# Kernel optimization log

Hardware: AMD Instinct MI355X
Metric: run time of the kernel (lower is better)

## Reference

```python
import jax, jax.numpy as jnp
import numpy as np

N_NODES = 100000
N_EDGES = 625000
D_IN = 128
D_HID = 256


def setup_inputs() -> dict:
    key = jax.random.key(0)
    ks = jax.random.split(key, 9)
    x = jax.random.normal(ks[0], (N_NODES, D_IN), dtype=jnp.float32)
    edge_index = jax.random.randint(ks[1], (2, N_EDGES), 0, N_NODES, dtype=jnp.int64)
    s = 1.0 / np.sqrt(D_IN)
    # SAGEConv params: lin_l applied to mean-aggregated neighbors (with bias),
    # lin_r applied to root features (no bias) -- PyG defaults.
    w_l = jax.random.uniform(ks[2], (D_IN, D_HID), minval=-s, maxval=s, dtype=jnp.float32)
    b_l = jax.random.uniform(ks[3], (D_HID,), minval=-s, maxval=s, dtype=jnp.float32)
    w_r = jax.random.uniform(ks[4], (D_IN, D_HID), minval=-s, maxval=s, dtype=jnp.float32)
    sh = 1.0 / np.sqrt(D_HID)
    w_p = jax.random.uniform(ks[5], (D_HID, 7), minval=-sh, maxval=sh, dtype=jnp.float32)
    b_p = jax.random.uniform(ks[6], (7,), minval=-sh, maxval=sh, dtype=jnp.float32)
    w_s = jax.random.uniform(ks[7], (D_HID, 6), minval=-sh, maxval=sh, dtype=jnp.float32)
    b_s = jax.random.uniform(ks[8], (6,), minval=-sh, maxval=sh, dtype=jnp.float32)
    return {"x": x, "edge_index": edge_index, "w_l": w_l, "b_l": b_l, "w_r": w_r,
            "w_p": w_p, "b_p": b_p, "w_s": w_s, "b_s": b_s}


def reference(x, edge_index, w_l, b_l, w_r, w_p, b_p, w_s, b_s):
    src, dst = edge_index[0], edge_index[1]
    n = x.shape[0]
    # SAGEConv mean aggregation: mean of source-node features over each target
    agg = jax.ops.segment_sum(x[src], dst, num_segments=n)          # [N, D_IN]
    cnt = jax.ops.segment_sum(jnp.ones(src.shape, x.dtype), dst, num_segments=n)
    mean = agg / jnp.maximum(cnt, 1.0)[:, None]                      # isolated nodes -> 0
    h = mean @ w_l + b_l + x @ w_r                                   # [N, D_HID]
    h = jax.nn.relu(h)                                               # dropout = identity (eval)
    pr = h @ w_p + b_p                                               # [N, 7]
    sv = h @ w_s + b_s                                               # [N, 6]
    return jax.nn.log_softmax(pr, axis=1), jax.nn.log_softmax(sv, axis=1)
```

## Files before the change

kernel.cpp:

```cpp
#include <hip/hip_runtime.h>
#include <hip/hip_bf16.h>
#include <math.h>

#define NN 100000
#define NE 625000
#define DIN 128
#define DH 256
#define NROWS 100096
#define CAP 32

#define HS_STRIDE 264

#define XCAST_BLOCKS 12500
#define EDGE_BLOCKS  2442
#define PACKW_BLOCKS 32
#define PACKH_BLOCKS 2
#define PREP_BLOCKS  (XCAST_BLOCKS + EDGE_BLOCKS + PACKW_BLOCKS + PACKH_BLOCKS)

typedef __attribute__((ext_vector_type(8))) short bf16x8;
typedef __attribute__((ext_vector_type(4))) float f32x4;

__device__ __forceinline__ unsigned short f2bf(float f) {
    unsigned u = __builtin_bit_cast(unsigned, f);
    u += 0x7fffu + ((u >> 16) & 1u);
    return (unsigned short)(u >> 16);
}
__device__ __forceinline__ float bflo(unsigned u) {
    return __builtin_bit_cast(float, u << 16);
}
__device__ __forceinline__ float bfhi(unsigned u) {
    return __builtin_bit_cast(float, u & 0xffff0000u);
}

__global__ __launch_bounds__(256)
void prep(const float* __restrict__ x, const int* __restrict__ ei,
          const float* __restrict__ w_l, const float* __restrict__ w_r,
          const float* __restrict__ w_p, const float* __restrict__ w_s,
          const float* __restrict__ b_p, const float* __restrict__ b_s,
          unsigned short* __restrict__ A, unsigned short* __restrict__ Bp,
          unsigned short* __restrict__ whp, float* __restrict__ bhc,
          int* __restrict__ deg, int* __restrict__ elist) {
    const int b = blockIdx.x;
    const int t = threadIdx.x;

    if (b < XCAST_BLOCKS) {
        int idx = b * 256 + t;
        int n = idx >> 5;
        int j4 = (idx & 31) * 4;
        float4 v = *reinterpret_cast<const float4*>(x + (size_t)n * DIN + j4);
        ushort4 o = { f2bf(v.x), f2bf(v.y), f2bf(v.z), f2bf(v.w) };
        *reinterpret_cast<ushort4*>(A + (size_t)n * 128 + j4) = o;
    } else if (b < XCAST_BLOCKS + EDGE_BLOCKS) {
        int e = (b - XCAST_BLOCKS) * 256 + t;
        if (e < NE) {
            int dst = ei[NE + e];
            int pos = atomicAdd(&deg[dst], 1);
            if (pos < CAP) elist[dst * CAP + pos] = ei[e];
        }
    } else if (b < XCAST_BLOCKS + EDGE_BLOCKS + PACKW_BLOCKS) {
        int tid = (b - XCAST_BLOCKS - EDGE_BLOCKS) * 256 + t;
        int kt = tid >> 10;
        int ct = (tid >> 6) & 15;
        int L = tid & 63;
        int k0 = kt * 32 + (L >> 4) * 8;
        int c = ct * 16 + (L & 15);
        unsigned short v[8];
#pragma unroll
        for (int j = 0; j < 8; ++j) {
            int k = k0 + j;
            float w = (k < 128) ? w_l[k * 256 + c] : w_r[(k - 128) * 256 + c];
            v[j] = f2bf(w);
        }
        int g = ((ct >> 3) << 6) + (kt << 3) + (ct & 7);
        *reinterpret_cast<bf16x8*>(Bp + (size_t)(g * 64 + L) * 8) =
            *reinterpret_cast<const bf16x8*>(v);
    } else {
        int tid = (b - XCAST_BLOCKS - EDGE_BLOCKS - PACKW_BLOCKS) * 256 + t;
        int kt = tid >> 6;
        int L = tid & 63;
        int k0 = kt * 32 + (L >> 4) * 8;
        int c = L & 15;
        unsigned short v[8];
#pragma unroll
        for (int j = 0; j < 8; ++j) {
            int k = k0 + j;
            float w = (c < 7) ? w_p[k * 7 + c] : (c < 13 ? w_s[k * 6 + (c - 7)] : 0.f);
            v[j] = f2bf(w);
        }
        *reinterpret_cast<bf16x8*>(whp + (size_t)tid * 8) =
            *reinterpret_cast<const bf16x8*>(v);
        if (tid < 16)
            bhc[tid] = (tid < 7) ? b_p[tid] : (tid < 13 ? b_s[tid - 7] : 0.f);
        if (tid >= 16 && tid < 32) {
            uint4 z = {0u, 0u, 0u, 0u};
            *reinterpret_cast<uint4*>(A + (size_t)NN * 128 + (tid - 16) * 8) = z;
        }
    }
}

__device__ __forceinline__ void gload(const unsigned short* __restrict__ A,
                                      int src, int q,
                                      uint4& v0, uint4& v1, uint4& v2, uint4& v3) {
    const unsigned short* xr = A + (size_t)src * 128 + q * 8;
    v0 = *reinterpret_cast<const uint4*>(xr);
    v1 = *reinterpret_cast<const uint4*>(xr + 32);
    v2 = *reinterpret_cast<const uint4*>(xr + 64);
    v3 = *reinterpret_cast<const uint4*>(xr + 96);
}

__device__ __forceinline__ void gacc(float* macc,
                                     const uint4& v0, const uint4& v1,
                                     const uint4& v2, const uint4& v3) {
    macc[0]  += bflo(v0.x); macc[1]  += bfhi(v0.x);
    macc[2]  += bflo(v0.y); macc[3]  += bfhi(v0.y);
    macc[4]  += bflo(v0.z); macc[5]  += bfhi(v0.z);
    macc[6]  += bflo(v0.w); macc[7]  += bfhi(v0.w);
    macc[8]  += bflo(v1.x); macc[9]  += bfhi(v1.x);
    macc[10] += bflo(v1.y); macc[11] += bfhi(v1.y);
    macc[12] += bflo(v1.z); macc[13] += bfhi(v1.z);
    macc[14] += bflo(v1.w); macc[15] += bfhi(v1.w);
    macc[16] += bflo(v2.x); macc[17] += bfhi(v2.x);
    macc[18] += bflo(v2.y); macc[19] += bfhi(v2.y);
    macc[20] += bflo(v2.z); macc[21] += bfhi(v2.z);
    macc[22] += bflo(v2.w); macc[23] += bfhi(v2.w);
    macc[24] += bflo(v3.x); macc[25] += bfhi(v3.x);
    macc[26] += bflo(v3.y); macc[27] += bfhi(v3.y);
    macc[28] += bflo(v3.z); macc[29] += bfhi(v3.z);
    macc[30] += bflo(v3.w); macc[31] += bfhi(v3.w);
}

__global__ __launch_bounds__(512, 4)
void sage_gemm_fused(const unsigned short* __restrict__ A,
                     const unsigned short* __restrict__ Bp,
                     const float* __restrict__ b_l,
                     const unsigned short* __restrict__ whp,
                     const float* __restrict__ bhc,
                     const int* __restrict__ elist,
                     const int* __restrict__ deg,
                     float* __restrict__ out) {
    __shared__ __align__(16) unsigned char smem[76288];
    unsigned short* Bs = (unsigned short*)smem;
    unsigned short* hs = (unsigned short*)smem;
    float* o13 = (float*)(smem + 67584);

    const int t = threadIdx.x;
    const int wave = t >> 6;
    const int L = t & 63;
    const int q = L >> 4;
    const int m15 = L & 15;
    const int node0 = blockIdx.x * 128;
    const int rowbase = node0 + wave * 16;
    const int n = rowbase + m15;

    {
        const uint4* gsrc = reinterpret_cast<const uint4*>(Bp);
        uint4* ldst = reinterpret_cast<uint4*>(Bs);
#pragma unroll
        for (int r = 0; r < 8; ++r)
            ldst[r * 512 + t] = gsrc[r * 512 + t];
    }

    const unsigned short* arow = A + (size_t)n * 128;
    bf16x8 afrag[8];
#pragma unroll
    for (int kt = 4; kt < 8; ++kt)
        afrag[kt] = *reinterpret_cast<const bf16x8*>(arow + (kt - 4) * 32 + q * 8);

    {
        float macc[32];
#pragma unroll
        for (int j = 0; j < 32; ++j) macc[j] = 0.f;
        int d = 0;
        if (n < NN) d = deg[n];
        const int dl = (d < CAP) ? d : CAP;
        const int dpad = (dl + 1) & ~1;
        const int base = (n < NN ? n : 0) * CAP;

        int s0 = elist[base + 0];
        int s1 = elist[base + 1];
        s0 = (dl > 0) ? s0 : NN;
        s1 = (dl > 1) ? s1 : NN;

        for (int i = 0; i < dpad; i += 2) {
            uint4 a0, a1, a2, a3, b0, b1, b2, b3;
            gload(A, s0, q, a0, a1, a2, a3);
            gload(A, s1, q, b0, b1, b2, b3);
            const int i2 = i + 2;
            int t0 = elist[base + (i2 & 31)];
            int t1 = elist[base + ((i2 + 1) & 31)];
            t0 = (i2 < dl) ? t0 : NN;
            t1 = (i2 + 1 < dl) ? t1 : NN;
            gacc(macc, a0, a1, a2, a3);
            gacc(macc, b0, b1, b2, b3);
            s0 = t0; s1 = t1;
        }

        const float invd = (d > 0) ? 1.f / (float)d : 0.f;
#pragma unroll
        for (int kt = 0; kt < 4; ++kt) {
            unsigned short vv[8];
#pragma unroll
            for (int j = 0; j < 8; ++j) vv[j] = f2bf(macc[kt * 8 + j] * invd);
            afrag[kt] = *reinterpret_cast<const bf16x8*>(vv);
        }
    }

    f32x4 acc[16];
#pragma unroll
    for (int ct = 0; ct < 16; ++ct) acc[ct] = (f32x4){0.f, 0.f, 0.f, 0.f};

    __syncthreads();

#pragma unroll
    for (int kt = 0; kt < 8; ++kt) {
#pragma unroll
        for (int c7 = 0; c7 < 8; ++c7) {
            bf16x8 b = *reinterpret_cast<const bf16x8*>(
                Bs + ((size_t)(kt * 8 + c7) * 64 + L) * 8);
            acc[c7] = __builtin_amdgcn_mfma_f32_16x16x32_bf16(afrag[kt], b, acc[c7], 0, 0, 0);
        }
    }

    __syncthreads();

    {
        const uint4* gsrc = reinterpret_cast<const uint4*>(Bp + 32768);
        uint4* ldst = reinterpret_cast<uint4*>(Bs);
#pragma unroll
        for (int r = 0; r < 8; ++r)
            ldst[r * 512 + t] = gsrc[r * 512 + t];
    }
    __syncthreads();

#pragma unroll
    for (int kt = 0; kt < 8; ++kt) {
#pragma unroll
        for (int c7 = 0; c7 < 8; ++c7) {
            bf16x8 b = *reinterpret_cast<const bf16x8*>(
                Bs + ((size_t)(kt * 8 + c7) * 64 + L) * 8);
            acc[8 + c7] = __builtin_amdgcn_mfma_f32_16x16x32_bf16(afrag[kt], b, acc[8 + c7], 0, 0, 0);
        }
    }

    __syncthreads();

#pragma unroll
    for (int ct = 0; ct < 16; ++ct) {
        const int c = ct * 16 + m15;
        const float blv = b_l[c];
        const int r0 = wave * 16 + q * 4;
#pragma unroll
        for (int r = 0; r < 4; ++r)
            hs[(r0 + r) * HS_STRIDE + c] = f2bf(fmaxf(acc[ct][r] + blv, 0.f));
    }
    __syncthreads();

    {
        f32x4 acch = (f32x4){0.f, 0.f, 0.f, 0.f};
        const unsigned short* hrow = hs + (size_t)(wave * 16 + m15) * HS_STRIDE;
#pragma unroll
        for (int kt = 0; kt < 8; ++kt) {
            bf16x8 ah = *reinterpret_cast<const bf16x8*>(hrow + kt * 32 + q * 8);
            bf16x8 bh = *reinterpret_cast<const bf16x8*>(whp + ((size_t)(kt * 64 + L)) * 8);
            acch = __builtin_amdgcn_mfma_f32_16x16x32_bf16(ah, bh, acch, 0, 0, 0);
        }
        if (m15 < 13) {
            const float bh = bhc[m15];
#pragma unroll
            for (int r = 0; r < 4; ++r)
                o13[(wave * 16 + q * 4 + r) * 17 + m15] = acch[r] + bh;
        }
    }
    __syncthreads();

    if (t < 128) {
        const int gnode = node0 + t;
        if (gnode < NN) {
            float v[7], mx = -1e30f;
#pragma unroll
            for (int j = 0; j < 7; ++j) { v[j] = o13[t * 17 + j]; mx = fmaxf(mx, v[j]); }
            float sum = 0.f;
#pragma unroll
            for (int j = 0; j < 7; ++j) sum += expf(v[j] - mx);
            const float lse = mx + logf(sum);
#pragma unroll
            for (int j = 0; j < 7; ++j) out[(size_t)gnode * 7 + j] = v[j] - lse;

            float u[6], mx2 = -1e30f;
#pragma unroll
            for (int j = 0; j < 6; ++j) { u[j] = o13[t * 17 + 7 + j]; mx2 = fmaxf(mx2, u[j]); }
            float sum2 = 0.f;
#pragma unroll
            for (int j = 0; j < 6; ++j) sum2 += expf(u[j] - mx2);
            const float lse2 = mx2 + logf(sum2);
#pragma unroll
            for (int j = 0; j < 6; ++j) out[(size_t)NN * 7 + (size_t)gnode * 6 + j] = u[j] - lse2;
        }
    }
}

extern "C" void kernel_launch(void* const* d_in, const int* in_sizes, int n_in,
                              void* d_out, int out_size, void* d_ws, size_t ws_size,
                              hipStream_t stream) {
    const float* x   = (const float*)d_in[0];
    const int*   ei  = (const int*)d_in[1];
    const float* w_l = (const float*)d_in[2];
    const float* b_l = (const float*)d_in[3];
    const float* w_r = (const float*)d_in[4];
    const float* w_p = (const float*)d_in[5];
    const float* b_p = (const float*)d_in[6];
    const float* w_s = (const float*)d_in[7];
    const float* b_s = (const float*)d_in[8];
    float* out = (float*)d_out;

    unsigned short* A   = (unsigned short*)d_ws;
    unsigned short* Bp  = A + (size_t)NROWS * 128;
    unsigned short* whp = Bp + 65536;
    float* bhc  = (float*)(whp + 4096);
    int* deg    = (int*)(bhc + 16);
    int* elist  = deg + NN;

    hipMemsetAsync(deg, 0, NN * sizeof(int), stream);

    prep<<<PREP_BLOCKS, 256, 0, stream>>>(x, ei, w_l, w_r, w_p, w_s, b_p, b_s,
                                          A, Bp, whp, bhc, deg, elist);

    sage_gemm_fused<<<NROWS / 128, 512, 0, stream>>>(A, Bp, b_l, whp, bhc,
                                                     elist, deg, out);
}
```

Measured before the change: 209.3 us.

## Counting-sort nodes by degree so each wave gathers neighbors of equal degree

Adds three small kernels that build a histogram of capped node degrees, a prefix scan and a scatter into a permutation that packs each node id with its capped degree. The fused gather+GEMM kernel then processes nodes in degree-sorted order, so the 16 nodes in a wave have near-equal neighbor counts and the gather loop wastes fewer iterations on lanes that have already finished. The cost is three extra launches, root-feature rows and output rows that are now read and written in scattered order, and a mean that divides by the capped degree instead of the true degree.

Result: slower. 220.5 us (+5.4%).

```diff
diff --git a/kernel.cpp b/kernel.cpp
--- a/kernel.cpp
+++ b/kernel.cpp
@@ -8,6 +8,7 @@
 #define DH 256
 #define NROWS 100096
 #define CAP 32
+#define NBINS 33
 
 #define HS_STRIDE 264
 
@@ -95,6 +96,60 @@
             uint4 z = {0u, 0u, 0u, 0u};
             *reinterpret_cast<uint4*>(A + (size_t)NN * 128 + (tid - 16) * 8) = z;
         }
+    }
+}
+
+__global__ __launch_bounds__(1024)
+void deg_hist(const int* __restrict__ deg, int* __restrict__ bins) {
+    __shared__ int h[NBINS];
+    const int t = threadIdx.x;
+    if (t < NBINS) h[t] = 0;
+    __syncthreads();
+    int n = blockIdx.x * 1024 + t;
+    if (n < NN) {
+        int d = deg[n];
+        int dl = (d < CAP) ? d : CAP;
+        atomicAdd(&h[dl], 1);
+    }
+    __syncthreads();
+    if (t < NBINS && h[t]) atomicAdd(&bins[t], h[t]);
+}
+
+__global__ __launch_bounds__(128)
+void deg_scan(const int* __restrict__ bins, int* __restrict__ cursor,
+              unsigned* __restrict__ perm) {
+    const int t = threadIdx.x;
+    if (t == 0) {
+        int run = 0;
+        for (int b = 0; b < NBINS; ++b) { cursor[b] = run; run += bins[b]; }
+    }
+    if (t >= 32) perm[NN + (t - 32)] = NN;
+}
+
+__global__ __launch_bounds__(1024)
+void deg_scatter(const int* __restrict__ deg, int* __restrict__ cursor,
+                 unsigned* __restrict__ perm) {
+    __shared__ int h[NBINS];
+    __shared__ int base[NBINS];
+    const int t = threadIdx.x;
+    const int n = blockIdx.x * 1024 + t;
+    if (t < NBINS) h[t] = 0;
+    __syncthreads();
+    int dl = 0;
+    if (n < NN) {
+        int d = deg[n];
+        dl = (d < CAP) ? d : CAP;
+        atomicAdd(&h[dl], 1);
+    }
+    __syncthreads();
+    if (t < NBINS) {
+        base[t] = h[t] ? atomicAdd(&cursor[t], h[t]) : 0;
+        h[t] = 0;
+    }
+    __syncthreads();
+    if (n < NN) {
+        int pos = base[dl] + atomicAdd(&h[dl], 1);
+        perm[pos] = (unsigned)n | ((unsigned)dl << 20);
     }
 }
 
@@ -136,7 +191,7 @@
                      const unsigned short* __restrict__ whp,
                      const float* __restrict__ bhc,
                      const int* __restrict__ elist,
-                     const int* __restrict__ deg,
+                     const unsigned* __restrict__ perm,
                      float* __restrict__ out) {
     __shared__ __align__(16) unsigned char smem[76288];
     unsigned short* Bs = (unsigned short*)smem;
@@ -150,17 +205,20 @@
     const int m15 = L & 15;
     const int node0 = blockIdx.x * 128;
     const int rowbase = node0 + wave * 16;
-    const int n = rowbase + m15;
+    const int r = rowbase + m15;
+    const unsigned pe = perm[r];
+    const int node = pe & 0xFFFFF;
+    const int dl = pe >> 20;
 
     {
         const uint4* gsrc = reinterpret_cast<const uint4*>(Bp);
         uint4* ldst = reinterpret_cast<uint4*>(Bs);
 #pragma unroll
-        for (int r = 0; r < 8; ++r)
-            ldst[r * 512 + t] = gsrc[r * 512 + t];
-    }
-
-    const unsigned short* arow = A + (size_t)n * 128;
+        for (int rr = 0; rr < 8; ++rr)
+            ldst[rr * 512 + t] = gsrc[rr * 512 + t];
+    }
+
+    const unsigned short* arow = A + (size_t)node * 128;
     bf16x8 afrag[8];
 #pragma unroll
     for (int kt = 4; kt < 8; ++kt)
@@ -170,11 +228,8 @@
         float macc[32];
 #pragma unroll
         for (int j = 0; j < 32; ++j) macc[j] = 0.f;
-        int d = 0;
-        if (n < NN) d = deg[n];
-        const int dl = (d < CAP) ? d : CAP;
         const int dpad = (dl + 1) & ~1;
-        const int base = (n < NN ? n : 0) * CAP;
+        const int base = (node < NN ? node : 0) * CAP;
 
         int s0 = elist[base + 0];
         int s1 = elist[base + 1];
@@ -195,7 +250,7 @@
             s0 = t0; s1 = t1;
         }
 
-        const float invd = (d > 0) ? 1.f / (float)d : 0.f;
+        const float invd = (dl > 0) ? 1.f / (float)dl : 0.f;
 #pragma unroll
         for (int kt = 0; kt < 4; ++kt) {
             unsigned short vv[8];
@@ -227,8 +282,8 @@
         const uint4* gsrc = reinterpret_cast<const uint4*>(Bp + 32768);
         uint4* ldst = reinterpret_cast<uint4*>(Bs);
 #pragma unroll
-        for (int r = 0; r < 8; ++r)
-            ldst[r * 512 + t] = gsrc[r * 512 + t];
+        for (int rr = 0; rr < 8; ++rr)
+            ldst[rr * 512 + t] = gsrc[rr * 512 + t];
     }
     __syncthreads();
 
@@ -250,8 +305,8 @@
         const float blv = b_l[c];
         const int r0 = wave * 16 + q * 4;
 #pragma unroll
-        for (int r = 0; r < 4; ++r)
-            hs[(r0 + r) * HS_STRIDE + c] = f2bf(fmaxf(acc[ct][r] + blv, 0.f));
+        for (int rr = 0; rr < 4; ++rr)
+            hs[(r0 + rr) * HS_STRIDE + c] = f2bf(fmaxf(acc[ct][rr] + blv, 0.f));
     }
     __syncthreads();
 
@@ -267,14 +322,15 @@
         if (m15 < 13) {
             const float bh = bhc[m15];
 #pragma unroll
-            for (int r = 0; r < 4; ++r)
-                o13[(wave * 16 + q * 4 + r) * 17 + m15] = acch[r] + bh;
+            for (int rr = 0; rr < 4; ++rr)
+                o13[(wave * 16 + q * 4 + rr) * 17 + m15] = acch[rr] + bh;
         }
     }
     __syncthreads();
 
     if (t < 128) {
-        const int gnode = node0 + t;
+        const unsigned pe2 = perm[node0 + t];
+        const int gnode = pe2 & 0xFFFFF;
         if (gnode < NN) {
             float v[7], mx = -1e30f;
 #pragma unroll
@@ -318,13 +374,20 @@
     unsigned short* whp = Bp + 65536;
     float* bhc  = (float*)(whp + 4096);
     int* deg    = (int*)(bhc + 16);
-    int* elist  = deg + NN;
-
-    hipMemsetAsync(deg, 0, NN * sizeof(int), stream);
+    int* bins   = deg + NN;
+    int* cursor = bins + 64;
+    int* elist  = cursor + 64;
+    unsigned* perm = (unsigned*)(elist + (size_t)NN * CAP);
+
+    hipMemsetAsync(deg, 0, (NN + 128) * sizeof(int), stream);
 
     prep<<<PREP_BLOCKS, 256, 0, stream>>>(x, ei, w_l, w_r, w_p, w_s, b_p, b_s,
                                           A, Bp, whp, bhc, deg, elist);
 
+    deg_hist<<<(NN + 1023) / 1024, 1024, 0, stream>>>(deg, bins);
+    deg_scan<<<1, 128, 0, stream>>>(bins, cursor, perm);
+    deg_scatter<<<(NN + 1023) / 1024, 1024, 0, stream>>>(deg, cursor, perm);
+
     sage_gemm_fused<<<NROWS / 128, 512, 0, stream>>>(A, Bp, b_l, whp, bhc,
-                                                     elist, deg, out);
-}
+                                                     elist, perm, out);
+}
```

## Split neighbor mean gather into separate kernel writing into widened A buffer

Applied to the files above, without the earlier changes.

Moves the neighbor-mean aggregation out of the fused GEMM kernel into a standalone gather_mean kernel with higher occupancy, storing bf16 means next to x in a stride-256 A buffer. The GEMM then simply loads both halves of the A row. This aims to improve latency hiding for the irregular gather, which was constrained by the GEMM kernel's large shared memory use, at the cost of an extra launch and an extra write/read of the mean matrix. Edge-list blocks are also reordered to run first in the prep grid.

New measurement: 251.3 us. +20.1%, slower.

```diff
diff --git a/kernel.cpp b/kernel.cpp
--- a/kernel.cpp
+++ b/kernel.cpp
@@ -8,14 +8,15 @@
 #define DH 256
 #define NROWS 100096
 #define CAP 32
+#define AST 256
 
 #define HS_STRIDE 264
 
+#define EDGE_BLOCKS  2442
 #define XCAST_BLOCKS 12500
-#define EDGE_BLOCKS  2442
 #define PACKW_BLOCKS 32
 #define PACKH_BLOCKS 2
-#define PREP_BLOCKS  (XCAST_BLOCKS + EDGE_BLOCKS + PACKW_BLOCKS + PACKH_BLOCKS)
+#define PREP_BLOCKS  (EDGE_BLOCKS + XCAST_BLOCKS + PACKW_BLOCKS + PACKH_BLOCKS)
 
 typedef __attribute__((ext_vector_type(8))) short bf16x8;
 typedef __attribute__((ext_vector_type(4))) float f32x4;
@@ -43,22 +44,22 @@
     const int b = blockIdx.x;
     const int t = threadIdx.x;
 
-    if (b < XCAST_BLOCKS) {
-        int idx = b * 256 + t;
+    if (b < EDGE_BLOCKS) {
+        int e = b * 256 + t;
+        if (e < NE) {
+            int dst = ei[NE + e];
+            int pos = atomicAdd(&deg[dst], 1);
+            if (pos < CAP) elist[dst * CAP + pos] = ei[e];
+        }
+    } else if (b < EDGE_BLOCKS + XCAST_BLOCKS) {
+        int idx = (b - EDGE_BLOCKS) * 256 + t;
         int n = idx >> 5;
         int j4 = (idx & 31) * 4;
         float4 v = *reinterpret_cast<const float4*>(x + (size_t)n * DIN + j4);
         ushort4 o = { f2bf(v.x), f2bf(v.y), f2bf(v.z), f2bf(v.w) };
-        *reinterpret_cast<ushort4*>(A + (size_t)n * 128 + j4) = o;
-    } else if (b < XCAST_BLOCKS + EDGE_BLOCKS) {
-        int e = (b - XCAST_BLOCKS) * 256 + t;
-        if (e < NE) {
-            int dst = ei[NE + e];
-            int pos = atomicAdd(&deg[dst], 1);
-            if (pos < CAP) elist[dst * CAP + pos] = ei[e];
-        }
-    } else if (b < XCAST_BLOCKS + EDGE_BLOCKS + PACKW_BLOCKS) {
-        int tid = (b - XCAST_BLOCKS - EDGE_BLOCKS) * 256 + t;
+        *reinterpret_cast<ushort4*>(A + (size_t)n * AST + 128 + j4) = o;
+    } else if (b < EDGE_BLOCKS + XCAST_BLOCKS + PACKW_BLOCKS) {
+        int tid = (b - EDGE_BLOCKS - XCAST_BLOCKS) * 256 + t;
         int kt = tid >> 10;
         int ct = (tid >> 6) & 15;
         int L = tid & 63;
@@ -75,7 +76,7 @@
         *reinterpret_cast<bf16x8*>(Bp + (size_t)(g * 64 + L) * 8) =
             *reinterpret_cast<const bf16x8*>(v);
     } else {
-        int tid = (b - XCAST_BLOCKS - EDGE_BLOCKS - PACKW_BLOCKS) * 256 + t;
+        int tid = (b - EDGE_BLOCKS - XCAST_BLOCKS - PACKW_BLOCKS) * 256 + t;
         int kt = tid >> 6;
         int L = tid & 63;
         int k0 = kt * 32 + (L >> 4) * 8;
@@ -93,7 +94,7 @@
             bhc[tid] = (tid < 7) ? b_p[tid] : (tid < 13 ? b_s[tid - 7] : 0.f);
         if (tid >= 16 && tid < 32) {
             uint4 z = {0u, 0u, 0u, 0u};
-            *reinterpret_cast<uint4*>(A + (size_t)NN * 128 + (tid - 16) * 8) = z;
+            *reinterpret_cast<uint4*>(A + (size_t)NN * AST + 128 + (tid - 16) * 8) = z;
         }
     }
 }
@@ -101,7 +102,7 @@
 __device__ __forceinline__ void gload(const unsigned short* __restrict__ A,
                                       int src, int q,
                                       uint4& v0, uint4& v1, uint4& v2, uint4& v3) {
-    const unsigned short* xr = A + (size_t)src * 128 + q * 8;
+    const unsigned short* xr = A + (size_t)src * AST + 128 + q * 8;
     v0 = *reinterpret_cast<const uint4*>(xr);
     v1 = *reinterpret_cast<const uint4*>(xr + 32);
     v2 = *reinterpret_cast<const uint4*>(xr + 64);
@@ -129,14 +130,65 @@
     macc[30] += bflo(v3.w); macc[31] += bfhi(v3.w);
 }
 
+__global__ __launch_bounds__(256, 6)
+void gather_mean(unsigned short* __restrict__ A,
+                 const int* __restrict__ elist,
+                 const int* __restrict__ deg) {
+    const int t = threadIdx.x;
+    const int L = t & 63;
+    const int q = L >> 4;
+    const int m15 = L & 15;
+    const int n = blockIdx.x * 64 + (t >> 6) * 16 + m15;
+
+    int d = 0;
+    if (n < NN) d = deg[n];
+    const int dl = (d < CAP) ? d : CAP;
+    const int dpad = (dl + 1) & ~1;
+    const int base = (n < NN ? n : 0) * CAP;
+
+    float macc[32];
+#pragma unroll
+    for (int j = 0; j < 32; ++j) macc[j] = 0.f;
+
+    int s0 = elist[base + 0];
+    int s1 = elist[base + 1];
+    s0 = (dl > 0) ? s0 : NN;
+    s1 = (dl > 1) ? s1 : NN;
+
+    for (int i = 0; i < dpad; i += 2) {
+        uint4 a0, a1, a2, a3, b0, b1, b2, b3;
+        gload(A, s0, q, a0, a1, a2, a3);
+        gload(A, s1, q, b0, b1, b2, b3);
+        const int i2 = i + 2;
+        int t0 = elist[base + (i2 & 31)];
+        int t1 = elist[base + ((i2 + 1) & 31)];
+        t0 = (i2 < dl) ? t0 : NN;
+        t1 = (i2 + 1 < dl) ? t1 : NN;
+        gacc(macc, a0, a1, a2, a3);
+        gacc(macc, b0, b1, b2, b3);
+        s0 = t0; s1 = t1;
+    }
+
+    if (n < NN) {
+        const float invd = (dl > 0) ? 1.f / (float)dl : 0.f;
+        unsigned short* mrow = A + (size_t)n * AST;
+#pragma unroll
+        for (int kt = 0; kt < 4; ++kt) {
+            unsigned short vv[8];
+#pragma unroll
+            for (int j = 0; j < 8; ++j) vv[j] = f2bf(macc[kt * 8 + j] * invd);
+            *reinterpret_cast<bf16x8*>(mrow + kt * 32 + q * 8) =
+                *reinterpret_cast<const bf16x8*>(vv);
+        }
+    }
+}
+
 __global__ __launch_bounds__(512, 4)
 void sage_gemm_fused(const unsigned short* __restrict__ A,
                      const unsigned short* __restrict__ Bp,
                      const float* __restrict__ b_l,
                      const unsigned short* __restrict__ whp,
                      const float* __restrict__ bhc,
-                     const int* __restrict__ elist,
-                     const int* __restrict__ deg,
                      float* __restrict__ out) {
     __shared__ __align__(16) unsigned char smem[76288];
     unsigned short* Bs = (unsigned short*)smem;
@@ -149,61 +201,21 @@
     const int q = L >> 4;
     const int m15 = L & 15;
     const int node0 = blockIdx.x * 128;
-    const int rowbase = node0 + wave * 16;
-    const int n = rowbase + m15;
+    const int node = node0 + wave * 16 + m15;
 
     {
         const uint4* gsrc = reinterpret_cast<const uint4*>(Bp);
         uint4* ldst = reinterpret_cast<uint4*>(Bs);
 #pragma unroll
-        for (int r = 0; r < 8; ++r)
-            ldst[r * 512 + t] = gsrc[r * 512 + t];
-    }
-
-    const unsigned short* arow = A + (size_t)n * 128;
+        for (int rr = 0; rr < 8; ++rr)
+            ldst[rr * 512 + t] = gsrc[rr * 512 + t];
+    }
+
+    const unsigned short* arow = A + (size_t)node * AST;
     bf16x8 afrag[8];
 #pragma unroll
-    for (int kt = 4; kt < 8; ++kt)
-        afrag[kt] = *reinterpret_cast<const bf16x8*>(arow + (kt - 4) * 32 + q * 8);
-
-    {
-        float macc[32];
-#pragma unroll
-        for (int j = 0; j < 32; ++j) macc[j] = 0.f;
-        int d = 0;
-        if (n < NN) d = deg[n];
-        const int dl = (d < CAP) ? d : CAP;
-        const int dpad = (dl + 1) & ~1;
-        const int base = (n < NN ? n : 0) * CAP;
-
-        int s0 = elist[base + 0];
-        int s1 = elist[base + 1];
-        s0 = (dl > 0) ? s0 : NN;
-        s1 = (dl > 1) ? s1 : NN;
-
-        for (int i = 0; i < dpad; i += 2) {
-            uint4 a0, a1, a2, a3, b0, b1, b2, b3;
-            gload(A, s0, q, a0, a1, a2, a3);
-            gload(A, s1, q, b0, b1, b2, b3);
-            const int i2 = i + 2;
-            int t0 = elist[base + (i2 & 31)];
-            int t1 = elist[base + ((i2 + 1) & 31)];
-            t0 = (i2 < dl) ? t0 : NN;
-            t1 = (i2 + 1 < dl) ? t1 : NN;
-            gacc(macc, a0, a1, a2, a3);
-            gacc(macc, b0, b1, b2, b3);
-            s0 = t0; s1 = t1;
-        }
-
-        const float invd = (d > 0) ? 1.f / (float)d : 0.f;
-#pragma unroll
-        for (int kt = 0; kt < 4; ++kt) {
-            unsigned short vv[8];
-#pragma unroll
-            for (int j = 0; j < 8; ++j) vv[j] = f2bf(macc[kt * 8 + j] * invd);
-            afrag[kt] = *reinterpret_cast<const bf16x8*>(vv);
-        }
-    }
+    for (int kt = 0; kt < 8; ++kt)
+        afrag[kt] = *reinterpret_cast<const bf16x8*>(arow + kt * 32 + q * 8);
 
     f32x4 acc[16];
 #pragma unroll
@@ -227,8 +239,8 @@
         const uint4* gsrc = reinterpret_cast<const uint4*>(Bp + 32768);
         uint4* ldst = reinterpret_cast<uint4*>(Bs);
 #pragma unroll
-        for (int r = 0; r < 8; ++r)
-            ldst[r * 512 + t] = gsrc[r * 512 + t];
+        for (int rr = 0; rr < 8; ++rr)
+            ldst[rr * 512 + t] = gsrc[rr * 512 + t];
     }
     __syncthreads();
 
@@ -250,8 +262,8 @@
         const float blv = b_l[c];
         const int r0 = wave * 16 + q * 4;
 #pragma unroll
-        for (int r = 0; r < 4; ++r)
-            hs[(r0 + r) * HS_STRIDE + c] = f2bf(fmaxf(acc[ct][r] + blv, 0.f));
+        for (int rr = 0; rr < 4; ++rr)
+            hs[(r0 + rr) * HS_STRIDE + c] = f2bf(fmaxf(acc[ct][rr] + blv, 0.f));
     }
     __syncthreads();
 
@@ -267,8 +279,8 @@
         if (m15 < 13) {
             const float bh = bhc[m15];
 #pragma unroll
-            for (int r = 0; r < 4; ++r)
-                o13[(wave * 16 + q * 4 + r) * 17 + m15] = acch[r] + bh;
+            for (int rr = 0; rr < 4; ++rr)
+                o13[(wave * 16 + q * 4 + rr) * 17 + m15] = acch[rr] + bh;
         }
     }
     __syncthreads();
@@ -314,7 +326,7 @@
     float* out = (float*)d_out;
 
     unsigned short* A   = (unsigned short*)d_ws;
-    unsigned short* Bp  = A + (size_t)NROWS * 128;
+    unsigned short* Bp  = A + (size_t)NROWS * AST;
     unsigned short* whp = Bp + 65536;
     float* bhc  = (float*)(whp + 4096);
     int* deg    = (int*)(bhc + 16);
@@ -325,6 +337,7 @@
     prep<<<PREP_BLOCKS, 256, 0, stream>>>(x, ei, w_l, w_r, w_p, w_s, b_p, b_s,
                                           A, Bp, whp, bhc, deg, elist);
 
-    sage_gemm_fused<<<NROWS / 128, 512, 0, stream>>>(A, Bp, b_l, whp, bhc,
-                                                     elist, deg, out);
-}
+    gather_mean<<<(NN + 63) / 64, 256, 0, stream>>>(A, elist, deg);
+
+    sage_gemm_fused<<<NROWS / 128, 512, 0, stream>>>(A, Bp, b_l, whp, bhc, out);
+}
```
